# Kernel optimization log

Hardware: AMD Instinct MI355X
Metric: run time of the kernel (lower is better)

Reference implementation:

```python
import jax, jax.numpy as jnp
import numpy as np

# irreps: input = 32x0e + 16x1o (dim 80); key/query/value = 8x0e + 4x1o (dim 20); lmax = 1
N_NODES = 10000
N_EDGES = 160000
MUL0_IN, MUL1_IN = 32, 16
MUL0_OUT, MUL1_OUT = 8, 4
NUM_BASIS = 32
HIDDEN = 32
MAX_RADIUS = 2.5
NUM_NEIGHBORS = 32
# per-edge fully-connected TP weight blocks (paths: 0e*0e->0e, 1o*1o->0e, 0e*1o->1o, 1o*0e->1o)
S00 = MUL0_IN * MUL0_OUT    # 256
S110 = MUL1_IN * MUL0_OUT   # 128
S01 = MUL0_IN * MUL1_OUT    # 128
S10 = MUL1_IN * MUL1_OUT    # 64
WNUMEL = S00 + S110 + S01 + S10  # 576
SQRT3 = 1.7320508075688772


def _split_irreps(z, mul0, mul1):
    return z[:, :mul0], z[:, mul0:].reshape(-1, mul1, 3)


def _basis_net(rb, w1, w2):
    # e3nn FullyConnectedNet([num_basis, 32, weight_numel], silu): x @ W / sqrt(fan_in)
    h = jax.nn.silu(rb @ w1 / jnp.sqrt(float(NUM_BASIS)))
    return h @ w2 / jnp.sqrt(float(HIDDEN))


def _edge_tp(x0, x1, Y1, w):
    # FullyConnectedTensorProduct with per-edge weights w [E, WNUMEL].
    # e3nn component/element normalization: path_weight = sqrt(dim(ir_out)/fan_in),
    # fan_in per output irrep = MUL0_IN + MUL1_IN = 48; CG(1,1,0)=CG(0,1,1)=delta/sqrt(3).
    c = 1.0 / jnp.sqrt(float(MUL0_IN + MUL1_IN))
    w00 = w[:, :S00].reshape(-1, MUL0_IN, MUL0_OUT)
    w110 = w[:, S00:S00 + S110].reshape(-1, MUL1_IN, MUL0_OUT)
    w01 = w[:, S00 + S110:S00 + S110 + S01].reshape(-1, MUL0_IN, MUL1_OUT)
    w10 = w[:, S00 + S110 + S01:].reshape(-1, MUL1_IN, MUL1_OUT)
    x1dotY = jnp.einsum('eum,em->eu', x1, Y1)  # [E, MUL1_IN]
    out0 = c * (jnp.einsum('euw,eu->ew', w00, x0)
                + jnp.einsum('euw,eu->ew', w110, x1dotY) / SQRT3)
    out1 = c * (jnp.einsum('euw,eu->ew', w01, x0)[:, :, None] * Y1[:, None, :]
                + jnp.einsum('euw,eum->ewm', w10, x1))
    return out0, out1  # [E, MUL0_OUT], [E, MUL1_OUT, 3]


def _forward(x, pos, w_q0, w_q1, w_kb1, w_kb2, w_vb1, w_vb2, w_sim0, w_sim1, edge_index):
    src, dst = edge_index[0], edge_index[1]
    vec = pos[src] - pos[dst]                                   # [E,3]
    r = jnp.sqrt(jnp.sum(vec * vec, axis=1) + 1e-24)            # [E]
    # bessel soft_one_hot_linspace (cutoff=True), scaled by sqrt(num_basis)
    n = jnp.arange(1, NUM_BASIS + 1, dtype=jnp.float32)
    rb = jnp.sqrt(2.0 / MAX_RADIUS) * jnp.sin(n * jnp.pi * r[:, None] / MAX_RADIUS) / r[:, None]
    rb = rb * jnp.sqrt(float(NUM_BASIS))
    # soft_unit_step(10*(1 - r/max_radius)) = exp(-1/t) for t > 0 else 0
    t = 10.0 * (1.0 - r / MAX_RADIUS)
    cutoff = jnp.where(t > 0.0, jnp.exp(-1.0 / jnp.maximum(t, 1e-12)), 0.0)
    # spherical harmonics lmax=1, 'component' norm: Y0 = 1, Y1 = sqrt(3)*unit_vec
    Y1 = SQRT3 * vec / r[:, None]
    x0, x1 = _split_irreps(x, MUL0_IN, MUL1_IN)
    # o3.Linear query projection: independent per-l blocks, / sqrt(fan_in)
    q0 = x0 @ w_q0 / jnp.sqrt(float(MUL0_IN))                   # [N,8]
    q1 = jnp.einsum('num,uw->nwm', x1, w_q1) / jnp.sqrt(float(MUL1_IN))  # [N,4,3]
    wk = _basis_net(rb, w_kb1, w_kb2)                           # [E,576]
    wv = _basis_net(rb, w_vb1, w_vb2)                           # [E,576]
    x0s, x1s = x0[src], x1[src]
    k0, k1 = _edge_tp(x0s, x1s, Y1, wk)
    v0, v1 = _edge_tp(x0s, x1s, Y1, wv)
    # similarity TP (query x key -> 0e): fan_in = 8*8 + 4*4 = 80
    cs = 1.0 / jnp.sqrt(float(MUL0_OUT ** 2 + MUL1_OUT ** 2))
    sim = cs * (jnp.einsum('uv,eu,ev->e', w_sim0, q0[src], k0)
                + jnp.einsum('uv,eum,evm->e', w_sim1, q1[src], k1) / SQRT3)
    logits = cutoff * sim
    # segment softmax grouped by src node
    m = jax.ops.segment_max(logits, src, num_segments=N_NODES)
    m = jnp.where(jnp.isfinite(m), m, 0.0)
    ex = jnp.exp(logits - m[src])
    den = jax.ops.segment_sum(ex, src, num_segments=N_NODES)
    attn = ex / den[src]                                        # [E]
    a = jnp.sqrt(jax.nn.relu(attn))[:, None]                    # [E,1]
    vals = jnp.concatenate([v0, v1.reshape(-1, MUL1_OUT * 3)], axis=1)  # [E,20]
    return jax.ops.segment_sum(a * vals, dst, num_segments=N_NODES) / NUM_NEIGHBORS


def setup_inputs():
    key = jax.random.key(0)
    ks = jax.random.split(key, 11)
    return {
        'x': jax.random.normal(ks[0], (N_NODES, MUL0_IN + 3 * MUL1_IN), jnp.float32),
        'pos': jax.random.uniform(ks[1], (N_NODES, 3), jnp.float32) * MAX_RADIUS,
        'w_q0': jax.random.normal(ks[2], (MUL0_IN, MUL0_OUT), jnp.float32),
        'w_q1': jax.random.normal(ks[3], (MUL1_IN, MUL1_OUT), jnp.float32),
        'w_kb1': jax.random.normal(ks[4], (NUM_BASIS, HIDDEN), jnp.float32),
        'w_kb2': jax.random.normal(ks[5], (HIDDEN, WNUMEL), jnp.float32),
        'w_vb1': jax.random.normal(ks[6], (NUM_BASIS, HIDDEN), jnp.float32),
        'w_vb2': jax.random.normal(ks[7], (HIDDEN, WNUMEL), jnp.float32),
        'w_sim0': jax.random.normal(ks[8], (MUL0_OUT, MUL0_OUT), jnp.float32),
        'w_sim1': jax.random.normal(ks[9], (MUL1_OUT, MUL1_OUT), jnp.float32),
        'edge_index': jax.random.randint(ks[10], (2, N_EDGES), 0, N_NODES, dtype=jnp.int32),
    }


def reference(x, pos, w_q0, w_q1, w_kb1, w_kb2, w_vb1, w_vb2, w_sim0, w_sim1, edge_index):
    return _forward(x, pos, w_q0, w_q1, w_kb1, w_kb2, w_vb1, w_vb2, w_sim0, w_sim1, edge_index)
```

## Files before the change

### kernel.cpp

```cpp
#include <hip/hip_runtime.h>
#include <hip/hip_fp16.h>
#include <math.h>

#define NN 10000
#define NE 160000

typedef _Float16 half8 __attribute__((ext_vector_type(8)));
typedef __attribute__((ext_vector_type(4))) float f32x4;

constexpr float SQRT3f    = 1.7320508075688772f;
constexpr float ISQRT3    = 0.57735026918962576f;
constexpr float ISQRT32   = 0.17677669529663687f;
constexpr float C_TP      = 0.14433756729740645f;
constexpr float CSIM      = 0.11180339887498949f;
constexpr float PREB      = 5.0596442562694074f;
constexpr float PI_OVER_R = 1.2566370614359172f;
constexpr float INV_RMAX  = 0.4f;
constexpr float HKSC      = C_TP * ISQRT32;
constexpr float DEN_SCALE = 16777216.0f;
constexpr float DEN_INV   = 1.0f / 16777216.0f;
constexpr float OUT_SCALE = 8388608.0f;
constexpr float OUT_INV   = 1.0f / 8388608.0f;

__device__ __forceinline__ unsigned fkey(float f) {
  unsigned u = __float_as_uint(f);
  return (u & 0x80000000u) ? ~u : (u | 0x80000000u);
}
__device__ __forceinline__ float funkey(unsigned k) {
  return (k & 0x80000000u) ? __uint_as_float(k ^ 0x80000000u)
                           : __uint_as_float(~k);
}
__device__ __forceinline__ unsigned short f2h(float f) {
  return __half_as_ushort(__float2half(f));
}

__device__ __forceinline__ int origcol(int n) {
  if (n >= 576) return 512 + (n - 576);
  int w = n / 48, u = n % 48;
  if (w < 8) return (u < 32) ? (u * 8 + w) : (256 + (u - 32) * 8 + w);
  return (u < 32) ? (384 + u * 4 + (w - 8)) : -1;
}

__global__ void __launch_bounds__(256) k_prep(
    const float* __restrict__ w_vb1, const float* __restrict__ w_vb2,
    float* __restrict__ W1vt, unsigned short* __restrict__ Wtv)
{
  int tid = blockIdx.x * 256 + threadIdx.x;
  if (tid < 640 * 32) {
    int n = tid / 32, h = tid % 32;
    int oc = origcol(n);
    float v = (oc >= 0) ? w_vb2[h * 576 + oc] : 0.0f;
    Wtv[n * 32 + h] = f2h(v);
  }
  if (tid < 1024) {
    int h = tid / 32, n2 = tid % 32;
    W1vt[h * 32 + n2] = w_vb1[n2 * 32 + h];
  }
}

__global__ void __launch_bounds__(256) k_node(
    const float* __restrict__ x, const float* __restrict__ w_q0,
    const float* __restrict__ w_q1, const float* __restrict__ w_sim0,
    const float* __restrict__ w_sim1,
    float* __restrict__ qs0, float* __restrict__ qs1)
{
  int n = blockIdx.x * 256 + threadIdx.x;
  if (n >= NN) return;
  float x0[32], x1f[48];
  const float4* xr = (const float4*)(x + 80 * n);
#pragma unroll
  for (int i = 0; i < 8; ++i) {
    float4 v = xr[i];
    x0[4*i]=v.x; x0[4*i+1]=v.y; x0[4*i+2]=v.z; x0[4*i+3]=v.w;
  }
#pragma unroll
  for (int i = 0; i < 12; ++i) {
    float4 v = xr[8 + i];
    x1f[4*i]=v.x; x1f[4*i+1]=v.y; x1f[4*i+2]=v.z; x1f[4*i+3]=v.w;
  }
  float q0[8];
#pragma unroll
  for (int w = 0; w < 8; ++w) {
    float a = 0.f;
#pragma unroll
    for (int u = 0; u < 32; ++u) a = fmaf(x0[u], w_q0[u * 8 + w], a);
    q0[w] = a * ISQRT32;
  }
  float q1[12];
#pragma unroll
  for (int w = 0; w < 4; ++w)
#pragma unroll
    for (int m = 0; m < 3; ++m) {
      float a = 0.f;
#pragma unroll
      for (int u = 0; u < 16; ++u) a = fmaf(x1f[3*u+m], w_q1[u*4+w], a);
      q1[w * 3 + m] = a * 0.25f;
    }
#pragma unroll
  for (int v = 0; v < 8; ++v) {
    float a = 0.f;
#pragma unroll
    for (int u = 0; u < 8; ++u) a = fmaf(w_sim0[u * 8 + v], q0[u], a);
    qs0[n * 8 + v] = CSIM * a;
  }
#pragma unroll
  for (int v = 0; v < 4; ++v)
#pragma unroll
    for (int m = 0; m < 3; ++m) {
      float a = 0.f;
#pragma unroll
      for (int u = 0; u < 4; ++u) a = fmaf(w_sim1[u*4+v], q1[u*3+m], a);
      qs1[n * 12 + v * 3 + m] = (CSIM * ISQRT3) * a;
    }
}

__global__ void __launch_bounds__(256) k_edge(
    const float* __restrict__ pos,
    const int* __restrict__ esrc, const int* __restrict__ edst,
    const float* __restrict__ W1vt,
    unsigned* __restrict__ hvo, float* __restrict__ geom,
    float* __restrict__ rbuf)
{
  int e = blockIdx.x * 256 + threadIdx.x;
  if (e >= NE) return;
  int s = esrc[e], d = edst[e];
  float vx = pos[3*s]   - pos[3*d];
  float vy = pos[3*s+1] - pos[3*d+1];
  float vz = pos[3*s+2] - pos[3*d+2];
  float r = sqrtf(fmaf(vx, vx, fmaf(vy, vy, vz * vz)) + 1e-24f);
  float inv_r = 1.0f / r;

  float rb[32];
  {
    float sn, cth;
    sincosf(PI_OVER_R * r, &sn, &cth);
    float twoc = 2.0f * cth, pre = PREB * inv_r, snm1 = 0.0f;
#pragma unroll
    for (int n = 0; n < 32; ++n) {
      rb[n] = pre * sn;
      float t = fmaf(twoc, sn, -snm1);
      snm1 = sn; sn = t;
    }
  }
  float Yx = SQRT3f * vx * inv_r, Yy = SQRT3f * vy * inv_r, Yz = SQRT3f * vz * inv_r;
  float tc = 10.0f * (1.0f - r * INV_RMAX);
  float cut = (tc > 0.0f) ? __expf(-1.0f / tc) : 0.0f;
  *(float4*)(geom + 4 * e) = make_float4(Yx, Yy, Yz, cut);
  rbuf[e] = r;

#pragma unroll 1
  for (int h = 0; h < 32; h += 2) {
    const float* wv0 = W1vt + h * 32;
    const float* wv1 = W1vt + (h + 1) * 32;
    float av0 = 0.f, av1 = 0.f;
#pragma unroll
    for (int n = 0; n < 32; ++n) {
      float rn = rb[n];
      av0 = fmaf(rn, wv0[n], av0);
      av1 = fmaf(rn, wv1[n], av1);
    }
    av0 *= ISQRT32; av1 *= ISQRT32;
    float hv0 = av0 / (1.0f + __expf(-av0)) * HKSC;
    float hv1 = av1 / (1.0f + __expf(-av1)) * HKSC;
    hvo[e * 16 + (h >> 1)] = (unsigned)f2h(hv0) | ((unsigned)f2h(hv1) << 16);
  }
}

template <int HALF>
__global__ void __launch_bounds__(256) k_nodeF(
    const float* __restrict__ x, const float* __restrict__ w_kb2,
    const float* __restrict__ qs0g, const float* __restrict__ qs1g,
    float* __restrict__ nodeF)
{
  __shared__ float W2f[16 * 577];
  __shared__ float ndl[16][100];

  const int tid = threadIdx.x;
  const int nb = blockIdx.x * 16;

#pragma unroll
  for (int i = 0; i < 36; ++i) {
    int idx = i * 256 + tid;
    int row = idx / 576, col = idx - row * 576;
    W2f[row * 577 + col] = w_kb2[(HALF * 16 + row) * 576 + col];
  }
  for (int j = tid; j < 1600; j += 256) {
    int nn = j / 100, jj = j - nn * 100;
    int n = nb + nn;
    float v;
    if (jj < 80)      v = x[80 * n + jj];
    else if (jj < 88) v = qs0g[8 * n + (jj - 80)];
    else              v = qs1g[12 * n + (jj - 88)];
    ndl[nn][jj] = v;
  }
  __syncthreads();

  const int nn = tid >> 4, hh = tid & 15;
  const float* Wh = W2f + hh * 577;
  const float* nd = ndl[nn];

  float t14 = 0.f;
#pragma unroll
  for (int a = 0; a < 32; ++a) {
    float tmp = 0.f;
#pragma unroll
    for (int v = 0; v < 8; ++v) tmp = fmaf(Wh[a * 8 + v], nd[80 + v], tmp);
    t14 = fmaf(tmp, nd[a], t14);
  }
#pragma unroll
  for (int a = 0; a < 16; ++a)
#pragma unroll
    for (int v = 0; v < 4; ++v) {
      float dotv = fmaf(nd[32 + 3*a], nd[88 + 3*v],
                   fmaf(nd[32 + 3*a + 1], nd[88 + 3*v + 1],
                        nd[32 + 3*a + 2] * nd[88 + 3*v + 2]));
      t14 = fmaf(Wh[512 + a * 4 + v], dotv, t14);
    }

  float F0 = 0.f, F1 = 0.f, F2 = 0.f;
#pragma unroll
  for (int a = 0; a < 16; ++a) {
    float q = 0.f;
#pragma unroll
    for (int v = 0; v < 8; ++v) q = fmaf(Wh[256 + a * 8 + v], nd[80 + v], q);
    F0 = fmaf(q, nd[32 + 3*a],     F0);
    F1 = fmaf(q, nd[32 + 3*a + 1], F1);
    F2 = fmaf(q, nd[32 + 3*a + 2], F2);
  }
  F0 *= ISQRT3; F1 *= ISQRT3; F2 *= ISQRT3;
#pragma unroll
  for (int v = 0; v < 4; ++v) {
    float rr = 0.f;
#pragma unroll
    for (int a = 0; a < 32; ++a) rr = fmaf(Wh[384 + a * 4 + v], nd[a], rr);
    F0 = fmaf(rr, nd[88 + 3*v],     F0);
    F1 = fmaf(rr, nd[88 + 3*v + 1], F1);
    F2 = fmaf(rr, nd[88 + 3*v + 2], F2);
  }

  const int n = nb + nn, h = HALF * 16 + hh;
  *(float4*)(nodeF + (size_t)(n * 32 + h) * 4) = make_float4(t14, F0, F1, F2);
}

__global__ void __launch_bounds__(256) k_elogit(
    const float* __restrict__ rbuf, const float* __restrict__ geom,
    const int* __restrict__ esrc, const float* __restrict__ w_kb1,
    const float* __restrict__ nodeF,
    float* __restrict__ logits, unsigned* __restrict__ mkey)
{
  __shared__ float W1s[32 * 33];
  const int tid = threadIdx.x;
#pragma unroll
  for (int i = 0; i < 4; ++i) {
    int idx = i * 256 + tid;
    W1s[(idx >> 5) * 33 + (idx & 31)] = w_kb1[idx];
  }
  __syncthreads();

  const int e = blockIdx.x * 256 + tid;
  if (e >= NE) return;
  const int s = esrc[e];
  const float r = rbuf[e];
  const float4 g4 = *(const float4*)(geom + 4 * e);

  float rb[32];
  {
    float sn, cth;
    sincosf(PI_OVER_R * r, &sn, &cth);
    float twoc = 2.0f * cth, pre = PREB / r, snm1 = 0.0f;
#pragma unroll
    for (int n = 0; n < 32; ++n) {
      rb[n] = pre * sn;
      float t = fmaf(twoc, sn, -snm1);
      snm1 = sn; sn = t;
    }
  }

  const float4* nf = (const float4*)(nodeF + (size_t)s * 128);
  float sim = 0.f;
#pragma unroll 1
  for (int h = 0; h < 32; ++h) {
    float ak = 0.f;
#pragma unroll
    for (int n = 0; n < 32; ++n) ak = fmaf(rb[n], W1s[n * 33 + h], ak);
    ak *= ISQRT32;
    float hk = ak / (1.0f + __expf(-ak)) * HKSC;
    float4 f = nf[h];
    float S = fmaf(f.y, g4.x, fmaf(f.z, g4.y, fmaf(f.w, g4.z, f.x)));
    sim = fmaf(hk, S, sim);
  }
  float lg = g4.w * sim;
  logits[e] = lg;
  atomicMax(mkey + s, fkey(lg));
}

__global__ void __launch_bounds__(256) k_den(
    const float* __restrict__ logits, const int* __restrict__ esrc,
    const unsigned* __restrict__ mkey,
    float* __restrict__ exb, int* __restrict__ deni)
{
  int e = blockIdx.x * 256 + threadIdx.x;
  if (e >= NE) return;
  int s = esrc[e];
  float m = funkey(mkey[s]);
  float ex = expf(logits[e] - m);
  exb[e] = ex;
  atomicAdd(&deni[s], __float2int_rn(ex * DEN_SCALE));
}

__global__ void __launch_bounds__(256) k_tpv(
    const unsigned short* __restrict__ hmat, const unsigned short* __restrict__ Wt,
    const float* __restrict__ x, const float* __restrict__ geom,
    const int* __restrict__ esrc, const int* __restrict__ edst,
    const float* __restrict__ exb, const int* __restrict__ deni,
    int* __restrict__ outi)
{
  __shared__ __align__(16) uint4  wlds4[2304];
  __shared__ __align__(16) float g_lds[4][16 * 52];
  __shared__ __align__(16) float x1_lds[4][16 * 52];

  const int l = threadIdx.x & 63, wv = threadIdx.x >> 6;
  const int tile = blockIdx.x * 4 + wv;
  const int G = l >> 4, c = l & 15;
  const int ebase = tile * 16;

  const uint4* Wt4 = (const uint4*)Wt;
#pragma unroll
  for (int i = 0; i < 9; ++i) {
    int chunk = i * 256 + threadIdx.x;
    wlds4[chunk] = Wt4[chunk];
  }

#pragma unroll
  for (int i = 0; i < 5; ++i) {
    int idx = i * 64 + l;
    int ee = idx / 20, q = idx - 20 * ee;
    int ss = esrc[ebase + ee];
    float4 v = *(const float4*)(x + 80 * ss + 4 * q);
    if (q < 8)
      *(float4*)(&g_lds[wv][ee * 52 + 4 * q]) = v;
    else
      *(float4*)(&x1_lds[wv][ee * 52 + 4 * q - 32]) = v;
  }
  {
    int ee = l >> 2, ug = l & 3;
    int ss = esrc[ebase + ee];
    float4 gm = *(const float4*)(geom + 4 * (ebase + ee));
    const float* xp = x + 80 * ss + 32 + 12 * ug;
    float4 p0 = *(const float4*)(xp);
    float4 p1 = *(const float4*)(xp + 4);
    float4 p2 = *(const float4*)(xp + 8);
    float4 o;
    o.x = ISQRT3 * fmaf(p0.x, gm.x, fmaf(p0.y, gm.y, p0.z * gm.z));
    o.y = ISQRT3 * fmaf(p0.w, gm.x, fmaf(p1.x, gm.y, p1.y * gm.z));
    o.z = ISQRT3 * fmaf(p1.z, gm.x, fmaf(p1.w, gm.y, p2.x * gm.z));
    o.w = ISQRT3 * fmaf(p2.y, gm.x, fmaf(p2.z, gm.y, p2.w * gm.z));
    *(float4*)(&g_lds[wv][ee * 52 + 32 + 4 * ug]) = o;
  }

  half8 a8 = *(const half8*)(hmat + (ebase + c) * 32 + 8 * G);

  __syncthreads();

  half8 bt[4];
#pragma unroll
  for (int t = 0; t < 4; ++t)
    bt[t] = *(const half8*)(Wt + ((36 + t) * 16 + c) * 32 + 8 * G);

  float vacc[4][12];
#pragma unroll
  for (int r = 0; r < 4; ++r)
#pragma unroll
    for (int w = 0; w < 12; ++w) vacc[r][w] = 0.0f;
  float ot1[4][3];
#pragma unroll
  for (int r = 0; r < 4; ++r) { ot1[r][0]=0.f; ot1[r][1]=0.f; ot1[r][2]=0.f; }

  const f32x4 zero4 = {0.f, 0.f, 0.f, 0.f};
#pragma unroll
  for (int t = 0; t < 36; ++t) {
    union { uint4 u; half8 h; } cvt;
    cvt.u = wlds4[(t * 16 + c) * 4 + G];
    f32x4 dd = __builtin_amdgcn_mfma_f32_16x16x32_f16(a8, cvt.h, zero4, 0, 0, 0);
    const int w = t / 3, u0 = (t % 3) * 16;
#pragma unroll
    for (int r = 0; r < 4; ++r)
      vacc[r][w] = fmaf(dd[r], g_lds[wv][(4 * G + r) * 52 + u0 + c], vacc[r][w]);
  }
#pragma unroll
  for (int t = 0; t < 4; ++t) {
    f32x4 dd = __builtin_amdgcn_mfma_f32_16x16x32_f16(a8, bt[t], zero4, 0, 0, 0);
    const int u = 4 * t + (c >> 2);
#pragma unroll
    for (int r = 0; r < 4; ++r) {
      const float* xp = &x1_lds[wv][(4 * G + r) * 52 + 3 * u];
      ot1[r][0] = fmaf(dd[r], xp[0], ot1[r][0]);
      ot1[r][1] = fmaf(dd[r], xp[1], ot1[r][1]);
      ot1[r][2] = fmaf(dd[r], xp[2], ot1[r][2]);
    }
  }

#pragma unroll
  for (int m = 1; m < 16; m <<= 1)
#pragma unroll
    for (int r = 0; r < 4; ++r)
#pragma unroll
      for (int w = 0; w < 12; ++w)
        vacc[r][w] += __shfl_xor(vacc[r][w], m);
#pragma unroll
  for (int m = 4; m < 16; m <<= 1)
#pragma unroll
    for (int r = 0; r < 4; ++r)
#pragma unroll
      for (int k = 0; k < 3; ++k)
        ot1[r][k] += __shfl_xor(ot1[r][k], m);

  float treg[4] = {0.f, 0.f, 0.f, 0.f};
#pragma unroll
  for (int w = 0; w < 12; ++w)
    if (c == w) {
#pragma unroll
      for (int r = 0; r < 4; ++r) treg[r] = vacc[r][w];
    }

  int sr[4]; float4 g4[4];
#pragma unroll
  for (int r = 0; r < 4; ++r) {
    sr[r] = esrc[ebase + 4 * G + r];
    g4[r] = *(const float4*)(geom + 4 * (ebase + 4 * G + r));
  }

  float a_[4]; int dst[4];
#pragma unroll
  for (int r = 0; r < 4; ++r) {
    int eg = ebase + 4 * G + r;
    dst[r] = edst[eg];
    float denf = (float)deni[sr[r]] * DEN_INV;
    a_[r] = sqrtf(fmaxf(exb[eg] / denf, 0.f)) * 0.03125f;
  }
  float s01w[4];
#pragma unroll
  for (int r = 0; r < 4; ++r) s01w[r] = __shfl_xor(treg[r], 8);
  if (c < 8) {
#pragma unroll
    for (int r = 0; r < 4; ++r)
      atomicAdd(outi + 20 * dst[r] + c,
                __float2int_rn(a_[r] * treg[r] * OUT_SCALE));
  }
  if (c < 4) {
#pragma unroll
    for (int r = 0; r < 4; ++r) {
      float vx_ = fmaf(s01w[r], g4[r].x, ot1[r][0]);
      float vy_ = fmaf(s01w[r], g4[r].y, ot1[r][1]);
      float vz_ = fmaf(s01w[r], g4[r].z, ot1[r][2]);
      atomicAdd(outi + 20 * dst[r] + 8 + 3 * c + 0,
                __float2int_rn(a_[r] * vx_ * OUT_SCALE));
      atomicAdd(outi + 20 * dst[r] + 8 + 3 * c + 1,
                __float2int_rn(a_[r] * vy_ * OUT_SCALE));
      atomicAdd(outi + 20 * dst[r] + 8 + 3 * c + 2,
                __float2int_rn(a_[r] * vz_ * OUT_SCALE));
    }
  }
}

__global__ void __launch_bounds__(256) k_out(
    const int* __restrict__ outi, float* __restrict__ out)
{
  int i = blockIdx.x * 256 + threadIdx.x;
  if (i < NN * 20) out[i] = (float)outi[i] * OUT_INV;
}

extern "C" void kernel_launch(void* const* d_in, const int* in_sizes, int n_in,
                              void* d_out, int out_size, void* d_ws, size_t ws_size,
                              hipStream_t stream)
{
  const float* x      = (const float*)d_in[0];
  const float* pos    = (const float*)d_in[1];
  const float* w_q0   = (const float*)d_in[2];
  const float* w_q1   = (const float*)d_in[3];
  const float* w_kb1  = (const float*)d_in[4];
  const float* w_kb2  = (const float*)d_in[5];
  const float* w_vb1  = (const float*)d_in[6];
  const float* w_vb2  = (const float*)d_in[7];
  const float* w_sim0 = (const float*)d_in[8];
  const float* w_sim1 = (const float*)d_in[9];
  const int*   eidx   = (const int*)d_in[10];
  const int* esrc = eidx;
  const int* edst = eidx + NE;
  float* out = (float*)d_out;

  float* ws      = (float*)d_ws;
  float* geom    = ws;
  float* rbuf    = geom + (size_t)NE * 4;
  float* qs0     = rbuf + NE;
  float* qs1     = qs0 + NN * 8;
  float* logits  = qs1 + NN * 12;
  float* exb     = logits + NE;
  float* W1vt    = exb + NE;
  float* nodeF   = W1vt + 1024;
  int*   deni    = (int*)(nodeF + (size_t)NN * 128);
  unsigned* mkey = (unsigned*)(deni + NN);
  int*   outi    = (int*)(mkey + NN);
  unsigned short* hv  = (unsigned short*)(outi + NN * 20);
  unsigned short* Wtv = hv + (size_t)NE * 32;

  hipMemsetAsync(deni, 0, (size_t)(NN * 22) * sizeof(int), stream);

  const int eb = (NE + 255) / 256;
  k_prep<<<dim3((640 * 32 + 255) / 256), dim3(256), 0, stream>>>(
      w_vb1, w_vb2, W1vt, Wtv);
  k_node<<<dim3((NN + 255) / 256), dim3(256), 0, stream>>>(
      x, w_q0, w_q1, w_sim0, w_sim1, qs0, qs1);
  k_edge<<<dim3(eb), dim3(256), 0, stream>>>(
      pos, esrc, edst, W1vt, (unsigned*)hv, geom, rbuf);
  k_nodeF<0><<<dim3(NN / 16), dim3(256), 0, stream>>>(
      x, w_kb2, qs0, qs1, nodeF);
  k_nodeF<1><<<dim3(NN / 16), dim3(256), 0, stream>>>(
      x, w_kb2, qs0, qs1, nodeF);
  k_elogit<<<dim3(eb), dim3(256), 0, stream>>>(
      rbuf, geom, esrc, w_kb1, nodeF, logits, mkey);
  k_den<<<dim3(eb), dim3(256), 0, stream>>>(logits, esrc, mkey, exb, deni);
  k_tpv<<<dim3(NE / 64), dim3(256), 0, stream>>>(
      hv, Wtv, x, geom, esrc, edst, exb, deni, outi);
  k_out<<<dim3((NN * 20 + 255) / 256), dim3(256), 0, stream>>>(outi, out);
}
```

Baseline: 184.5 us.

## Fuse edge hidden and logit kernels; restructure value TP as gated MFMA contraction

Merges the edge geometry/value-hidden kernel with the key-logit kernel, so the Bessel basis is computed once and the key weights are transposed in the prep kernel. The value tensor product in k_tpv now folds the per-edge node features into the MFMA A operand and contracts over hidden×input channels, with accumulation inside the MFMA. This removes the per-output FMA epilogue and the long shuffle reductions. The value hidden buffer is stored in fp32 instead of fp16, which doubles its memory traffic, and the A operands are now built with packed fp16 conversions.

```diff
diff --git a/kernel.cpp b/kernel.cpp
--- a/kernel.cpp
+++ b/kernel.cpp
@@ -5,6 +5,7 @@
 #define NN 10000
 #define NE 160000
 
+typedef _Float16 half2v __attribute__((ext_vector_type(2)));
 typedef _Float16 half8 __attribute__((ext_vector_type(8)));
 typedef __attribute__((ext_vector_type(4))) float f32x4;
 
@@ -33,28 +34,61 @@
 __device__ __forceinline__ unsigned short f2h(float f) {
   return __half_as_ushort(__float2half(f));
 }
-
-__device__ __forceinline__ int origcol(int n) {
-  if (n >= 576) return 512 + (n - 576);
-  int w = n / 48, u = n % 48;
-  if (w < 8) return (u < 32) ? (u * 8 + w) : (256 + (u - 32) * 8 + w);
-  return (u < 32) ? (384 + u * 4 + (w - 8)) : -1;
+__device__ __forceinline__ half2v pk2(float a, float b) {
+#if defined(__has_builtin) && __has_builtin(__builtin_amdgcn_cvt_pkrtz)
+  auto t = __builtin_amdgcn_cvt_pkrtz(a, b);
+  half2v r; r[0] = t[0]; r[1] = t[1];
+  return r;
+#else
+  half2v r; r[0] = (_Float16)a; r[1] = (_Float16)b;
+  return r;
+#endif
+}
+__device__ __forceinline__ half8 mk_a(float4 h4, float g0, float g1) {
+  union { half2v h2[4]; half8 h8; } u;
+  u.h2[0] = pk2(h4.x * g0, h4.x * g1);
+  u.h2[1] = pk2(h4.y * g0, h4.y * g1);
+  u.h2[2] = pk2(h4.z * g0, h4.z * g1);
+  u.h2[3] = pk2(h4.w * g0, h4.w * g1);
+  return u.h8;
 }
 
 __global__ void __launch_bounds__(256) k_prep(
     const float* __restrict__ w_vb1, const float* __restrict__ w_vb2,
-    float* __restrict__ W1vt, unsigned short* __restrict__ Wtv)
+    const float* __restrict__ w_kb1,
+    float* __restrict__ W1vt, float* __restrict__ W1kt,
+    unsigned short* __restrict__ Btg)
 {
   int tid = blockIdx.x * 256 + threadIdx.x;
-  if (tid < 640 * 32) {
-    int n = tid / 32, h = tid % 32;
-    int oc = origcol(n);
-    float v = (oc >= 0) ? w_vb2[h * 576 + oc] : 0.0f;
-    Wtv[n * 32 + h] = f2h(v);
-  }
-  if (tid < 1024) {
-    int h = tid / 32, n2 = tid % 32;
-    W1vt[h * 32 + n2] = w_vb1[n2 * 32 + h];
+  if (tid < 12288) {
+    int t = tid / 384, rem = tid % 384;
+    int w = rem >> 5, k = rem & 31;
+    int uq = t >> 1, H = t & 1;
+    int h = 16 * H + (k >> 1), u = 2 * uq + (k & 1);
+    int oc = (w < 8) ? (u * 8 + w) : (384 + u * 4 + (w - 8));
+    Btg[tid] = f2h(w_vb2[h * 576 + oc]);
+  } else if (tid < 16384) {
+    int j = tid - 12288;
+    int t = j >> 8, rem = j & 255;
+    int w = rem >> 5, k = rem & 31;
+    int uq = 16 + (t >> 1), H = t & 1;
+    int h = 16 * H + (k >> 1), u = 2 * uq + (k & 1);
+    Btg[tid] = f2h(w_vb2[h * 576 + 256 + (u - 32) * 8 + w]);
+  } else if (tid < 18432) {
+    int j = tid - 16384;
+    int t = j >> 7, rem = j & 127;
+    int w = rem >> 5, k = rem & 31;
+    int up = t >> 1, H = t & 1;
+    int h = 16 * H + (k >> 1), u2 = 2 * up + (k & 1);
+    Btg[tid] = f2h(w_vb2[h * 576 + 512 + u2 * 4 + w]);
+  } else if (tid < 19456) {
+    int j = tid - 18432;
+    int h = j >> 5, n = j & 31;
+    W1vt[h * 32 + n] = w_vb1[n * 32 + h];
+  } else if (tid < 20480) {
+    int j = tid - 19456;
+    int h = j >> 5, n = j & 31;
+    W1kt[h * 32 + n] = w_kb1[n * 32 + h];
   }
 }
 
@@ -114,12 +148,90 @@
     }
 }
 
-__global__ void __launch_bounds__(256) k_edge(
+template <int HALF>
+__global__ void __launch_bounds__(256) k_nodeF(
+    const float* __restrict__ x, const float* __restrict__ w_kb2,
+    const float* __restrict__ qs0g, const float* __restrict__ qs1g,
+    float* __restrict__ nodeF)
+{
+  __shared__ float W2f[16 * 577];
+  __shared__ float ndl[16][100];
+
+  const int tid = threadIdx.x;
+  const int nb = blockIdx.x * 16;
+
+#pragma unroll
+  for (int i = 0; i < 36; ++i) {
+    int idx = i * 256 + tid;
+    int row = idx / 576, col = idx - row * 576;
+    W2f[row * 577 + col] = w_kb2[(HALF * 16 + row) * 576 + col];
+  }
+  for (int j = tid; j < 1600; j += 256) {
+    int nn = j / 100, jj = j - nn * 100;
+    int n = nb + nn;
+    float v;
+    if (jj < 80)      v = x[80 * n + jj];
+    else if (jj < 88) v = qs0g[8 * n + (jj - 80)];
+    else              v = qs1g[12 * n + (jj - 88)];
+    ndl[nn][jj] = v;
+  }
+  __syncthreads();
+
+  const int nn = tid >> 4, hh = tid & 15;
+  const float* Wh = W2f + hh * 577;
+  const float* nd = ndl[nn];
+
+  float t14 = 0.f;
+#pragma unroll
+  for (int a = 0; a < 32; ++a) {
+    float tmp = 0.f;
+#pragma unroll
+    for (int v = 0; v < 8; ++v) tmp = fmaf(Wh[a * 8 + v], nd[80 + v], tmp);
+    t14 = fmaf(tmp, nd[a], t14);
+  }
+#pragma unroll
+  for (int a = 0; a < 16; ++a)
+#pragma unroll
+    for (int v = 0; v < 4; ++v) {
+      float dotv = fmaf(nd[32 + 3*a], nd[88 + 3*v],
+                   fmaf(nd[32 + 3*a + 1], nd[88 + 3*v + 1],
+                        nd[32 + 3*a + 2] * nd[88 + 3*v + 2]));
+      t14 = fmaf(Wh[512 + a * 4 + v], dotv, t14);
+    }
+
+  float F0 = 0.f, F1 = 0.f, F2 = 0.f;
+#pragma unroll
+  for (int a = 0; a < 16; ++a) {
+    float q = 0.f;
+#pragma unroll
+    for (int v = 0; v < 8; ++v) q = fmaf(Wh[256 + a * 8 + v], nd[80 + v], q);
+    F0 = fmaf(q, nd[32 + 3*a],     F0);
+    F1 = fmaf(q, nd[32 + 3*a + 1], F1);
+    F2 = fmaf(q, nd[32 + 3*a + 2], F2);
+  }
+  F0 *= ISQRT3; F1 *= ISQRT3; F2 *= ISQRT3;
+#pragma unroll
+  for (int v = 0; v < 4; ++v) {
+    float rr = 0.f;
+#pragma unroll
+    for (int a = 0; a < 32; ++a) rr = fmaf(Wh[384 + a * 4 + v], nd[a], rr);
+    F0 = fmaf(rr, nd[88 + 3*v],     F0);
+    F1 = fmaf(rr, nd[88 + 3*v + 1], F1);
+    F2 = fmaf(rr, nd[88 + 3*v + 2], F2);
+  }
+
+  const int n = nb + nn, h = HALF * 16 + hh;
+  *(float4*)(nodeF + (size_t)(n * 32 + h) * 4) = make_float4(t14, F0, F1, F2);
+}
+
+__global__ void __launch_bounds__(256) k_edgelogit(
     const float* __restrict__ pos,
     const int* __restrict__ esrc, const int* __restrict__ edst,
-    const float* __restrict__ W1vt,
-    unsigned* __restrict__ hvo, float* __restrict__ geom,
-    float* __restrict__ rbuf)
+    const float* __restrict__ W1vt, const float* __restrict__ W1kt,
+    const float* __restrict__ nodeF,
+    float* __restrict__ hv, float* __restrict__ geom,
+    float* __restrict__ rbuf,
+    float* __restrict__ logits, unsigned* __restrict__ mkey)
 {
   int e = blockIdx.x * 256 + threadIdx.x;
   if (e >= NE) return;
@@ -148,148 +260,27 @@
   *(float4*)(geom + 4 * e) = make_float4(Yx, Yy, Yz, cut);
   rbuf[e] = r;
 
-#pragma unroll 1
-  for (int h = 0; h < 32; h += 2) {
-    const float* wv0 = W1vt + h * 32;
-    const float* wv1 = W1vt + (h + 1) * 32;
-    float av0 = 0.f, av1 = 0.f;
-#pragma unroll
-    for (int n = 0; n < 32; ++n) {
-      float rn = rb[n];
-      av0 = fmaf(rn, wv0[n], av0);
-      av1 = fmaf(rn, wv1[n], av1);
-    }
-    av0 *= ISQRT32; av1 *= ISQRT32;
-    float hv0 = av0 / (1.0f + __expf(-av0)) * HKSC;
-    float hv1 = av1 / (1.0f + __expf(-av1)) * HKSC;
-    hvo[e * 16 + (h >> 1)] = (unsigned)f2h(hv0) | ((unsigned)f2h(hv1) << 16);
-  }
-}
-
-template <int HALF>
-__global__ void __launch_bounds__(256) k_nodeF(
-    const float* __restrict__ x, const float* __restrict__ w_kb2,
-    const float* __restrict__ qs0g, const float* __restrict__ qs1g,
-    float* __restrict__ nodeF)
-{
-  __shared__ float W2f[16 * 577];
-  __shared__ float ndl[16][100];
-
-  const int tid = threadIdx.x;
-  const int nb = blockIdx.x * 16;
-
-#pragma unroll
-  for (int i = 0; i < 36; ++i) {
-    int idx = i * 256 + tid;
-    int row = idx / 576, col = idx - row * 576;
-    W2f[row * 577 + col] = w_kb2[(HALF * 16 + row) * 576 + col];
-  }
-  for (int j = tid; j < 1600; j += 256) {
-    int nn = j / 100, jj = j - nn * 100;
-    int n = nb + nn;
-    float v;
-    if (jj < 80)      v = x[80 * n + jj];
-    else if (jj < 88) v = qs0g[8 * n + (jj - 80)];
-    else              v = qs1g[12 * n + (jj - 88)];
-    ndl[nn][jj] = v;
-  }
-  __syncthreads();
-
-  const int nn = tid >> 4, hh = tid & 15;
-  const float* Wh = W2f + hh * 577;
-  const float* nd = ndl[nn];
-
-  float t14 = 0.f;
-#pragma unroll
-  for (int a = 0; a < 32; ++a) {
-    float tmp = 0.f;
-#pragma unroll
-    for (int v = 0; v < 8; ++v) tmp = fmaf(Wh[a * 8 + v], nd[80 + v], tmp);
-    t14 = fmaf(tmp, nd[a], t14);
-  }
-#pragma unroll
-  for (int a = 0; a < 16; ++a)
-#pragma unroll
-    for (int v = 0; v < 4; ++v) {
-      float dotv = fmaf(nd[32 + 3*a], nd[88 + 3*v],
-                   fmaf(nd[32 + 3*a + 1], nd[88 + 3*v + 1],
-                        nd[32 + 3*a + 2] * nd[88 + 3*v + 2]));
-      t14 = fmaf(Wh[512 + a * 4 + v], dotv, t14);
-    }
-
-  float F0 = 0.f, F1 = 0.f, F2 = 0.f;
-#pragma unroll
-  for (int a = 0; a < 16; ++a) {
-    float q = 0.f;
-#pragma unroll
-    for (int v = 0; v < 8; ++v) q = fmaf(Wh[256 + a * 8 + v], nd[80 + v], q);
-    F0 = fmaf(q, nd[32 + 3*a],     F0);
-    F1 = fmaf(q, nd[32 + 3*a + 1], F1);
-    F2 = fmaf(q, nd[32 + 3*a + 2], F2);
-  }
-  F0 *= ISQRT3; F1 *= ISQRT3; F2 *= ISQRT3;
-#pragma unroll
-  for (int v = 0; v < 4; ++v) {
-    float rr = 0.f;
-#pragma unroll
-    for (int a = 0; a < 32; ++a) rr = fmaf(Wh[384 + a * 4 + v], nd[a], rr);
-    F0 = fmaf(rr, nd[88 + 3*v],     F0);
-    F1 = fmaf(rr, nd[88 + 3*v + 1], F1);
-    F2 = fmaf(rr, nd[88 + 3*v + 2], F2);
-  }
-
-  const int n = nb + nn, h = HALF * 16 + hh;
-  *(float4*)(nodeF + (size_t)(n * 32 + h) * 4) = make_float4(t14, F0, F1, F2);
-}
-
-__global__ void __launch_bounds__(256) k_elogit(
-    const float* __restrict__ rbuf, const float* __restrict__ geom,
-    const int* __restrict__ esrc, const float* __restrict__ w_kb1,
-    const float* __restrict__ nodeF,
-    float* __restrict__ logits, unsigned* __restrict__ mkey)
-{
-  __shared__ float W1s[32 * 33];
-  const int tid = threadIdx.x;
-#pragma unroll
-  for (int i = 0; i < 4; ++i) {
-    int idx = i * 256 + tid;
-    W1s[(idx >> 5) * 33 + (idx & 31)] = w_kb1[idx];
-  }
-  __syncthreads();
-
-  const int e = blockIdx.x * 256 + tid;
-  if (e >= NE) return;
-  const int s = esrc[e];
-  const float r = rbuf[e];
-  const float4 g4 = *(const float4*)(geom + 4 * e);
-
-  float rb[32];
-  {
-    float sn, cth;
-    sincosf(PI_OVER_R * r, &sn, &cth);
-    float twoc = 2.0f * cth, pre = PREB / r, snm1 = 0.0f;
-#pragma unroll
-    for (int n = 0; n < 32; ++n) {
-      rb[n] = pre * sn;
-      float t = fmaf(twoc, sn, -snm1);
-      snm1 = sn; sn = t;
-    }
-  }
-
-  const float4* nf = (const float4*)(nodeF + (size_t)s * 128);
+  const float4* nf = (const float4*)(nodeF) + (size_t)s * 32;
   float sim = 0.f;
 #pragma unroll 1
   for (int h = 0; h < 32; ++h) {
-    float ak = 0.f;
-#pragma unroll
-    for (int n = 0; n < 32; ++n) ak = fmaf(rb[n], W1s[n * 33 + h], ak);
-    ak *= ISQRT32;
+    const float* wvp = W1vt + h * 32;
+    const float* wkp = W1kt + h * 32;
+    float av = 0.f, ak = 0.f;
+#pragma unroll
+    for (int n = 0; n < 32; ++n) {
+      av = fmaf(rb[n], wvp[n], av);
+      ak = fmaf(rb[n], wkp[n], ak);
+    }
+    av *= ISQRT32; ak *= ISQRT32;
+    float hvv = av / (1.0f + __expf(-av)) * HKSC;
+    hv[(size_t)e * 32 + h] = hvv;
     float hk = ak / (1.0f + __expf(-ak)) * HKSC;
     float4 f = nf[h];
-    float S = fmaf(f.y, g4.x, fmaf(f.z, g4.y, fmaf(f.w, g4.z, f.x)));
+    float S = fmaf(f.y, Yx, fmaf(f.z, Yy, fmaf(f.w, Yz, f.x)));
     sim = fmaf(hk, S, sim);
   }
-  float lg = g4.w * sim;
+  float lg = cut * sim;
   logits[e] = lg;
   atomicMax(mkey + s, fkey(lg));
 }
@@ -309,38 +300,35 @@
 }
 
 __global__ void __launch_bounds__(256) k_tpv(
-    const unsigned short* __restrict__ hmat, const unsigned short* __restrict__ Wt,
+    const float* __restrict__ hv, const unsigned short* __restrict__ Btg,
     const float* __restrict__ x, const float* __restrict__ geom,
     const int* __restrict__ esrc, const int* __restrict__ edst,
     const float* __restrict__ exb, const int* __restrict__ deni,
     int* __restrict__ outi)
 {
-  __shared__ __align__(16) uint4  wlds4[2304];
-  __shared__ __align__(16) float g_lds[4][16 * 52];
-  __shared__ __align__(16) float x1_lds[4][16 * 52];
+  __shared__ __align__(16) unsigned short Bls[18432];
+  __shared__ __align__(16) float g_lds[4][832];
+  __shared__ __align__(16) float x1_lds[4][832];
 
   const int l = threadIdx.x & 63, wv = threadIdx.x >> 6;
-  const int tile = blockIdx.x * 4 + wv;
   const int G = l >> 4, c = l & 15;
-  const int ebase = tile * 16;
-
-  const uint4* Wt4 = (const uint4*)Wt;
-#pragma unroll
-  for (int i = 0; i < 9; ++i) {
-    int chunk = i * 256 + threadIdx.x;
-    wlds4[chunk] = Wt4[chunk];
-  }
-
+  const int ebase = (blockIdx.x * 4 + wv) * 16;
+
+  {
+    const uint4* src = (const uint4*)Btg;
+    uint4* dst4 = (uint4*)Bls;
+#pragma unroll
+    for (int i = 0; i < 9; ++i)
+      dst4[i * 256 + threadIdx.x] = src[i * 256 + threadIdx.x];
+  }
 #pragma unroll
   for (int i = 0; i < 5; ++i) {
     int idx = i * 64 + l;
     int ee = idx / 20, q = idx - 20 * ee;
     int ss = esrc[ebase + ee];
     float4 v = *(const float4*)(x + 80 * ss + 4 * q);
-    if (q < 8)
-      *(float4*)(&g_lds[wv][ee * 52 + 4 * q]) = v;
-    else
-      *(float4*)(&x1_lds[wv][ee * 52 + 4 * q - 32]) = v;
+    if (q < 8) *(float4*)(&g_lds[wv][ee * 52 + 4 * q]) = v;
+    else       *(float4*)(&x1_lds[wv][ee * 52 + 4 * q - 32]) = v;
   }
   {
     int ee = l >> 2, ug = l & 3;
@@ -357,102 +345,94 @@
     o.w = ISQRT3 * fmaf(p2.y, gm.x, fmaf(p2.z, gm.y, p2.w * gm.z));
     *(float4*)(&g_lds[wv][ee * 52 + 32 + 4 * ug]) = o;
   }
-
-  half8 a8 = *(const half8*)(hmat + (ebase + c) * 32 + 8 * G);
+  const float4* hp = (const float4*)(hv + (size_t)(ebase + c) * 32);
+  float4 hA = hp[G];
+  float4 hB = hp[4 + G];
 
   __syncthreads();
 
-  half8 bt[4];
-#pragma unroll
-  for (int t = 0; t < 4; ++t)
-    bt[t] = *(const half8*)(Wt + ((36 + t) * 16 + c) * 32 + 8 * G);
-
-  float vacc[4][12];
-#pragma unroll
-  for (int r = 0; r < 4; ++r)
-#pragma unroll
-    for (int w = 0; w < 12; ++w) vacc[r][w] = 0.0f;
-  float ot1[4][3];
-#pragma unroll
-  for (int r = 0; r < 4; ++r) { ot1[r][0]=0.f; ot1[r][1]=0.f; ot1[r][2]=0.f; }
-
-  const f32x4 zero4 = {0.f, 0.f, 0.f, 0.f};
-#pragma unroll
-  for (int t = 0; t < 36; ++t) {
-    union { uint4 u; half8 h; } cvt;
-    cvt.u = wlds4[(t * 16 + c) * 4 + G];
-    f32x4 dd = __builtin_amdgcn_mfma_f32_16x16x32_f16(a8, cvt.h, zero4, 0, 0, 0);
-    const int w = t / 3, u0 = (t % 3) * 16;
-#pragma unroll
-    for (int r = 0; r < 4; ++r)
-      vacc[r][w] = fmaf(dd[r], g_lds[wv][(4 * G + r) * 52 + u0 + c], vacc[r][w]);
-  }
-#pragma unroll
-  for (int t = 0; t < 4; ++t) {
-    f32x4 dd = __builtin_amdgcn_mfma_f32_16x16x32_f16(a8, bt[t], zero4, 0, 0, 0);
-    const int u = 4 * t + (c >> 2);
-#pragma unroll
-    for (int r = 0; r < 4; ++r) {
-      const float* xp = &x1_lds[wv][(4 * G + r) * 52 + 3 * u];
-      ot1[r][0] = fmaf(dd[r], xp[0], ot1[r][0]);
-      ot1[r][1] = fmaf(dd[r], xp[1], ot1[r][1]);
-      ot1[r][2] = fmaf(dd[r], xp[2], ot1[r][2]);
-    }
-  }
-
-#pragma unroll
-  for (int m = 1; m < 16; m <<= 1)
-#pragma unroll
-    for (int r = 0; r < 4; ++r)
-#pragma unroll
-      for (int w = 0; w < 12; ++w)
-        vacc[r][w] += __shfl_xor(vacc[r][w], m);
-#pragma unroll
-  for (int m = 4; m < 16; m <<= 1)
-#pragma unroll
-    for (int r = 0; r < 4; ++r)
-#pragma unroll
-      for (int k = 0; k < 3; ++k)
-        ot1[r][k] += __shfl_xor(ot1[r][k], m);
-
-  float treg[4] = {0.f, 0.f, 0.f, 0.f};
-#pragma unroll
-  for (int w = 0; w < 12; ++w)
-    if (c == w) {
-#pragma unroll
-      for (int r = 0; r < 4; ++r) treg[r] = vacc[r][w];
-    }
-
-  int sr[4]; float4 g4[4];
+  const int cw12 = min(c, 11) * 32;
+  const int cw8  = min(c, 7) * 32;
+  const int cw4  = min(c, 3) * 32;
+  const float* gl = &g_lds[wv][c * 52];
+  const float* xl = &x1_lds[wv][c * 52];
+
+  f32x4 accA = {0.f,0.f,0.f,0.f}, accB = {0.f,0.f,0.f,0.f};
+  f32x4 accC = {0.f,0.f,0.f,0.f}, accD = {0.f,0.f,0.f,0.f};
+  f32x4 am0  = {0.f,0.f,0.f,0.f}, am1  = {0.f,0.f,0.f,0.f}, am2 = {0.f,0.f,0.f,0.f};
+
+#pragma unroll
+  for (int uq = 0; uq < 16; ++uq) {
+    float g0 = gl[2 * uq], g1 = gl[2 * uq + 1];
+    half8 a0 = mk_a(hA, g0, g1);
+    half8 a1 = mk_a(hB, g0, g1);
+    half8 b0 = *(const half8*)(Bls + (uq * 2    ) * 384 + cw12 + 8 * G);
+    half8 b1 = *(const half8*)(Bls + (uq * 2 + 1) * 384 + cw12 + 8 * G);
+    accA = __builtin_amdgcn_mfma_f32_16x16x32_f16(a0, b0, accA, 0, 0, 0);
+    accB = __builtin_amdgcn_mfma_f32_16x16x32_f16(a1, b1, accB, 0, 0, 0);
+  }
+#pragma unroll
+  for (int uq = 0; uq < 8; ++uq) {
+    float g0 = gl[32 + 2 * uq], g1 = gl[32 + 2 * uq + 1];
+    half8 a0 = mk_a(hA, g0, g1);
+    half8 a1 = mk_a(hB, g0, g1);
+    half8 b0 = *(const half8*)(Bls + 12288 + (uq * 2    ) * 256 + cw8 + 8 * G);
+    half8 b1 = *(const half8*)(Bls + 12288 + (uq * 2 + 1) * 256 + cw8 + 8 * G);
+    accC = __builtin_amdgcn_mfma_f32_16x16x32_f16(a0, b0, accC, 0, 0, 0);
+    accD = __builtin_amdgcn_mfma_f32_16x16x32_f16(a1, b1, accD, 0, 0, 0);
+  }
+#pragma unroll
+  for (int up = 0; up < 8; ++up) {
+    half8 b0 = *(const half8*)(Bls + 16384 + (up * 2    ) * 128 + cw4 + 8 * G);
+    half8 b1 = *(const half8*)(Bls + 16384 + (up * 2 + 1) * 128 + cw4 + 8 * G);
+    {
+      float xa = xl[6 * up + 0], xb = xl[6 * up + 3];
+      am0 = __builtin_amdgcn_mfma_f32_16x16x32_f16(mk_a(hA, xa, xb), b0, am0, 0, 0, 0);
+      am0 = __builtin_amdgcn_mfma_f32_16x16x32_f16(mk_a(hB, xa, xb), b1, am0, 0, 0, 0);
+    }
+    {
+      float xa = xl[6 * up + 1], xb = xl[6 * up + 4];
+      am1 = __builtin_amdgcn_mfma_f32_16x16x32_f16(mk_a(hA, xa, xb), b0, am1, 0, 0, 0);
+      am1 = __builtin_amdgcn_mfma_f32_16x16x32_f16(mk_a(hB, xa, xb), b1, am1, 0, 0, 0);
+    }
+    {
+      float xa = xl[6 * up + 2], xb = xl[6 * up + 5];
+      am2 = __builtin_amdgcn_mfma_f32_16x16x32_f16(mk_a(hA, xa, xb), b0, am2, 0, 0, 0);
+      am2 = __builtin_amdgcn_mfma_f32_16x16x32_f16(mk_a(hB, xa, xb), b1, am2, 0, 0, 0);
+    }
+  }
+
+  float tsum[4], out0v[4], s01w[4];
 #pragma unroll
   for (int r = 0; r < 4; ++r) {
-    sr[r] = esrc[ebase + 4 * G + r];
-    g4[r] = *(const float4*)(geom + 4 * (ebase + 4 * G + r));
-  }
-
-  float a_[4]; int dst[4];
+    tsum[r]  = accA[r] + accB[r];
+    out0v[r] = tsum[r] + accC[r] + accD[r];
+  }
+#pragma unroll
+  for (int r = 0; r < 4; ++r) s01w[r] = __shfl_xor(tsum[r], 8);
+
+  int sr[4], dst[4]; float4 g4[4]; float a_[4];
 #pragma unroll
   for (int r = 0; r < 4; ++r) {
     int eg = ebase + 4 * G + r;
+    sr[r] = esrc[eg];
     dst[r] = edst[eg];
+    g4[r] = *(const float4*)(geom + 4 * eg);
     float denf = (float)deni[sr[r]] * DEN_INV;
     a_[r] = sqrtf(fmaxf(exb[eg] / denf, 0.f)) * 0.03125f;
   }
-  float s01w[4];
-#pragma unroll
-  for (int r = 0; r < 4; ++r) s01w[r] = __shfl_xor(treg[r], 8);
   if (c < 8) {
 #pragma unroll
     for (int r = 0; r < 4; ++r)
       atomicAdd(outi + 20 * dst[r] + c,
-                __float2int_rn(a_[r] * treg[r] * OUT_SCALE));
+                __float2int_rn(a_[r] * out0v[r] * OUT_SCALE));
   }
   if (c < 4) {
 #pragma unroll
     for (int r = 0; r < 4; ++r) {
-      float vx_ = fmaf(s01w[r], g4[r].x, ot1[r][0]);
-      float vy_ = fmaf(s01w[r], g4[r].y, ot1[r][1]);
-      float vz_ = fmaf(s01w[r], g4[r].z, ot1[r][2]);
+      float vx_ = fmaf(s01w[r], g4[r].x, am0[r]);
+      float vy_ = fmaf(s01w[r], g4[r].y, am1[r]);
+      float vz_ = fmaf(s01w[r], g4[r].z, am2[r]);
       atomicAdd(outi + 20 * dst[r] + 8 + 3 * c + 0,
                 __float2int_rn(a_[r] * vx_ * OUT_SCALE));
       atomicAdd(outi + 20 * dst[r] + 8 + 3 * c + 1,
@@ -496,31 +476,30 @@
   float* qs1     = qs0 + NN * 8;
   float* logits  = qs1 + NN * 12;
   float* exb     = logits + NE;
-  float* W1vt    = exb + NE;
-  float* nodeF   = W1vt + 1024;
+  float* nodeF   = exb + NE;
   int*   deni    = (int*)(nodeF + (size_t)NN * 128);
   unsigned* mkey = (unsigned*)(deni + NN);
   int*   outi    = (int*)(mkey + NN);
-  unsigned short* hv  = (unsigned short*)(outi + NN * 20);
-  unsigned short* Wtv = hv + (size_t)NE * 32;
+  float* W1vt    = (float*)(outi + NN * 20);
+  float* W1kt    = W1vt + 1024;
+  float* hv      = W1kt + 1024;
+  unsigned short* Btg = (unsigned short*)(hv + (size_t)NE * 32);
 
   hipMemsetAsync(deni, 0, (size_t)(NN * 22) * sizeof(int), stream);
 
   const int eb = (NE + 255) / 256;
-  k_prep<<<dim3((640 * 32 + 255) / 256), dim3(256), 0, stream>>>(
-      w_vb1, w_vb2, W1vt, Wtv);
+  k_prep<<<dim3(80), dim3(256), 0, stream>>>(
+      w_vb1, w_vb2, w_kb1, W1vt, W1kt, Btg);
   k_node<<<dim3((NN + 255) / 256), dim3(256), 0, stream>>>(
       x, w_q0, w_q1, w_sim0, w_sim1, qs0, qs1);
-  k_edge<<<dim3(eb), dim3(256), 0, stream>>>(
-      pos, esrc, edst, W1vt, (unsigned*)hv, geom, rbuf);
   k_nodeF<0><<<dim3(NN / 16), dim3(256), 0, stream>>>(
       x, w_kb2, qs0, qs1, nodeF);
   k_nodeF<1><<<dim3(NN / 16), dim3(256), 0, stream>>>(
       x, w_kb2, qs0, qs1, nodeF);
-  k_elogit<<<dim3(eb), dim3(256), 0, stream>>>(
-      rbuf, geom, esrc, w_kb1, nodeF, logits, mkey);
+  k_edgelogit<<<dim3(eb), dim3(256), 0, stream>>>(
+      pos, esrc, edst, W1vt, W1kt, nodeF, hv, geom, rbuf, logits, mkey);
   k_den<<<dim3(eb), dim3(256), 0, stream>>>(logits, esrc, mkey, exb, deni);
   k_tpv<<<dim3(NE / 64), dim3(256), 0, stream>>>(
-      hv, Wtv, x, geom, esrc, edst, exb, deni, outi);
+      hv, Btg, x, geom, esrc, edst, exb, deni, outi);
   k_out<<<dim3((NN * 20 + 255) / 256), dim3(256), 0, stream>>>(outi, out);
 }
```

Measured after the change: 237.1 us. 28.5% more time.
